# Kernel optimization log

Measured on AMD Instinct MI355X. Metric: run time of the kernel, lower is better.

## Reference

```python
import jax, jax.numpy as jnp
import numpy as np

N_NODES = 65536
N_EDGES = 524288
FEAT_DIM = 512
EMBED_DIM = 512


def setup_inputs() -> dict:
    key = jax.random.key(0)
    k1, k2, k3, k4, k5 = jax.random.split(key, 5)
    x = jax.random.normal(k1, (N_NODES, FEAT_DIM), dtype=jnp.float32)
    # xavier_uniform for (embed_dim, feat_dim)
    limit = float(np.sqrt(6.0 / (EMBED_DIM + FEAT_DIM)))
    weight = jax.random.uniform(k2, (EMBED_DIM, FEAT_DIM), dtype=jnp.float32,
                                minval=-limit, maxval=limit)
    row = jax.random.randint(k3, (N_EDGES,), 0, N_NODES, dtype=jnp.int64)
    col = jax.random.randint(k4, (N_EDGES,), 0, N_NODES, dtype=jnp.int64)
    vals = jax.random.uniform(k5, (N_EDGES,), dtype=jnp.float32)
    return {"x": x, "weight": weight, "row": row, "col": col, "vals": vals}


def reference(x, weight, row, col, vals):
    # Fused GEMM + SpMM: out = adj @ (x @ weight.T)
    h = jnp.einsum('nf,ef->ne', x, weight)            # [N, embed_dim] dense GEMM
    msgs = vals[:, None] * h[col]                     # [E, embed_dim] gather + scale
    out = jax.ops.segment_sum(msgs, row, num_segments=N_NODES)  # SpMM scatter-add
    return out
```

## Files before the change

kernel.cpp:

```cpp
#include <hip/hip_runtime.h>
#include <stdint.h>


#define N_NODES 65536
#define N_EDGES 524288
#define FEAT    512
#define EMB     512
#define CAP     64

typedef short  short8  __attribute__((ext_vector_type(8)));
typedef float  floatx4 __attribute__((ext_vector_type(4)));
typedef unsigned int uintx2 __attribute__((ext_vector_type(2)));

__device__ __forceinline__ unsigned short f2bf(float f) {
    unsigned int u = __float_as_uint(f);
    u += 0x7FFFu + ((u >> 16) & 1u);
    return (unsigned short)(u >> 16);
}
__device__ __forceinline__ float bf2f_lo(unsigned int u){ return __uint_as_float(u << 16); }
__device__ __forceinline__ float bf2f_hi(unsigned int u){ return __uint_as_float(u & 0xffff0000u); }

typedef __attribute__((address_space(1))) const void* gas_vp;
typedef __attribute__((address_space(3))) void*       las_vp;
#define GLDS16(g, l) __builtin_amdgcn_global_load_lds((gas_vp)(const void*)(g), (las_vp)(void*)(l), 16, 0, 0)

__global__ __launch_bounds__(256)
void conv_bf16(const float* __restrict__ in, unsigned short* __restrict__ out)
{
    size_t i = ((size_t)blockIdx.x * 256 + threadIdx.x) * 8;
    floatx4 a = __builtin_nontemporal_load((const floatx4*)&in[i]);
    floatx4 b = __builtin_nontemporal_load((const floatx4*)&in[i + 4]);
    ushort4 lo, hi;
    lo.x = f2bf(a.x); lo.y = f2bf(a.y); lo.z = f2bf(a.z); lo.w = f2bf(a.w);
    hi.x = f2bf(b.x); hi.y = f2bf(b.y); hi.z = f2bf(b.z); hi.w = f2bf(b.w);
    *(ushort4*)&out[i]     = lo;
    *(ushort4*)&out[i + 4] = hi;
}

__global__ __launch_bounds__(256)
void gemm_fast(const unsigned short* __restrict__ xb, const unsigned short* __restrict__ wb,
               unsigned short* __restrict__ h)
{
    __shared__ unsigned short As[128 * 64];
    __shared__ unsigned short Bs[128 * 64];

    const int t    = threadIdx.x;
    const int lane = t & 63;
    const int wave = t >> 6;
    const int wm   = wave >> 1;
    const int wn   = wave & 1;
    const int l15  = lane & 15;
    const int lq   = lane >> 4;

    const int xcd = blockIdx.x & 7;
    const int loc = blockIdx.x >> 3;
    const int m0  = (xcd * 64 + (loc >> 2)) * 128;
    const int n0  = (loc & 3) * 128;

    floatx4 acc[4][4];
    #pragma unroll
    for (int i = 0; i < 4; i++)
        #pragma unroll
        for (int j = 0; j < 4; j++) acc[i][j] = (floatx4){0.f, 0.f, 0.f, 0.f};

    const int r8 = t >> 3;
    const int c8 = t & 7;

    for (int kb = 0; kb < FEAT; kb += 64) {
        #pragma unroll
        for (int p = 0; p < 4; p++) {
            int row = p * 32 + r8;
            int lc  = c8 ^ (row & 7);
            GLDS16(&xb[(m0 + row) * FEAT + kb + lc * 8], &As[row * 64 + c8 * 8]);
            GLDS16(&wb[(n0 + row) * FEAT + kb + lc * 8], &Bs[row * 64 + c8 * 8]);
        }
        __syncthreads();
        #pragma unroll
        for (int kk = 0; kk < 2; kk++) {
            short8 af[4], bf[4];
            #pragma unroll
            for (int mt = 0; mt < 4; mt++) {
                int r  = wm * 64 + mt * 16 + l15;
                int pc = (kk * 4 + lq) ^ (r & 7);
                af[mt] = *(const short8*)&As[r * 64 + pc * 8];
            }
            #pragma unroll
            for (int nt = 0; nt < 4; nt++) {
                int r  = wn * 64 + nt * 16 + l15;
                int pc = (kk * 4 + lq) ^ (r & 7);
                bf[nt] = *(const short8*)&Bs[r * 64 + pc * 8];
            }
            #pragma unroll
            for (int mt = 0; mt < 4; mt++)
                #pragma unroll
                for (int nt = 0; nt < 4; nt++)
                    acc[mt][nt] = __builtin_amdgcn_mfma_f32_16x16x32_bf16(
                        af[mt], bf[nt], acc[mt][nt], 0, 0, 0);
        }
        __syncthreads();
    }

    #pragma unroll
    for (int mt = 0; mt < 4; mt++)
        #pragma unroll
        for (int nt = 0; nt < 4; nt++)
            #pragma unroll
            for (int r = 0; r < 4; r++) {
                int row = m0 + wm * 64 + mt * 16 + lq * 4 + r;
                int col = n0 + wn * 64 + nt * 16 + l15;
                h[row * EMB + col] = f2bf(acc[mt][nt][r]);
            }
}

#define BM 128
#define BN 64
#define LDA 72

__global__ __launch_bounds__(256)
void gemm_f32(const float* __restrict__ x, const float* __restrict__ w,
              unsigned short* __restrict__ h)
{
    __shared__ unsigned short As[BM][LDA];
    __shared__ unsigned short Bs[BN][LDA];

    const int t = threadIdx.x, lane = t & 63, wave = t >> 6;
    const int wm = wave >> 1, wn = wave & 1;
    const int l15 = lane & 15, lq = lane >> 4;
    const int xcd = blockIdx.x & 7;
    const int loc = blockIdx.x >> 3;
    const int m0 = (xcd * 64 + (loc >> 3)) * BM;
    const int n0 = (loc & 7) * BN;

    floatx4 acc[4][2];
    #pragma unroll
    for (int i = 0; i < 4; i++)
        #pragma unroll
        for (int j = 0; j < 2; j++) acc[i][j] = (floatx4){0.f, 0.f, 0.f, 0.f};

    for (int kb = 0; kb < FEAT; kb += 64) {
        #pragma unroll
        for (int p = 0; p < 8; p++) {
            int idx = p * 256 + t, row = idx >> 4, cv = (idx & 15) << 2;
            float4 v = *(const float4*)&x[(m0 + row) * FEAT + kb + cv];
            ushort4 b4 = {f2bf(v.x), f2bf(v.y), f2bf(v.z), f2bf(v.w)};
            *(ushort4*)&As[row][cv] = b4;
        }
        #pragma unroll
        for (int p = 0; p < 4; p++) {
            int idx = p * 256 + t, row = idx >> 4, cv = (idx & 15) << 2;
            float4 v = *(const float4*)&w[(n0 + row) * FEAT + kb + cv];
            ushort4 b4 = {f2bf(v.x), f2bf(v.y), f2bf(v.z), f2bf(v.w)};
            *(ushort4*)&Bs[row][cv] = b4;
        }
        __syncthreads();
        #pragma unroll
        for (int kk = 0; kk < 2; kk++) {
            short8 af[4], bf[2];
            #pragma unroll
            for (int mt = 0; mt < 4; mt++)
                af[mt] = *(const short8*)&As[wm * 64 + mt * 16 + l15][kk * 32 + lq * 8];
            #pragma unroll
            for (int nt = 0; nt < 2; nt++)
                bf[nt] = *(const short8*)&Bs[wn * 32 + nt * 16 + l15][kk * 32 + lq * 8];
            #pragma unroll
            for (int mt = 0; mt < 4; mt++)
                #pragma unroll
                for (int nt = 0; nt < 2; nt++)
                    acc[mt][nt] = __builtin_amdgcn_mfma_f32_16x16x32_bf16(
                        af[mt], bf[nt], acc[mt][nt], 0, 0, 0);
        }
        __syncthreads();
    }
    #pragma unroll
    for (int mt = 0; mt < 4; mt++)
        #pragma unroll
        for (int nt = 0; nt < 2; nt++)
            #pragma unroll
            for (int r = 0; r < 4; r++) {
                int row = m0 + wm * 64 + mt * 16 + lq * 4 + r;
                int col = n0 + wn * 32 + nt * 16 + l15;
                h[row * EMB + col] = f2bf(acc[mt][nt][r]);
            }
}

__global__ __launch_bounds__(256)
void fill_edges(const int* __restrict__ row, const int* __restrict__ col,
                const float* __restrict__ vals, int* __restrict__ cnt,
                uintx2* __restrict__ ebuf)
{
    int e = blockIdx.x * 256 + threadIdx.x;
    int   r = __builtin_nontemporal_load(&row[e]);
    int   c = __builtin_nontemporal_load(&col[e]);
    float v = __builtin_nontemporal_load(&vals[e]);
    int slot = atomicAdd(&cnt[r], 1);
    if (slot < CAP) {
        uintx2 ev; ev.x = (unsigned)c; ev.y = __float_as_uint(v);
        ebuf[r * CAP + slot] = ev;
    }
}

__global__ __launch_bounds__(256)
void rowsum(const unsigned short* __restrict__ h, const int* __restrict__ cnt,
            const uintx2* __restrict__ ebuf, float* __restrict__ out)
{
    const int r    = blockIdx.x * 4 + (threadIdx.x >> 6);
    const int lane = threadIdx.x & 63;
    int deg = cnt[r];
    if (deg > CAP) deg = CAP;
    const int base = r * CAP;

    int   c_l = 0;
    float v_l = 0.f;
    if (lane < deg) {
        uintx2 ev = ebuf[base + lane];
        c_l = (int)ev.x;
        v_l = __uint_as_float(ev.y);
    }

    float acc[8] = {0.f,0.f,0.f,0.f,0.f,0.f,0.f,0.f};
    for (int i0 = 0; i0 < deg; i0 += 8) {
        uint4 hv[8]; float vv[8];
        int nn = deg - i0; if (nn > 8) nn = 8;
        #pragma unroll
        for (int j = 0; j < 8; j++) {
            if (j < nn) {
                int c = __shfl(c_l, i0 + j, 64);
                vv[j] = __shfl(v_l, i0 + j, 64);
                hv[j] = *(const uint4*)&h[c * EMB + lane * 8];
            }
        }
        #pragma unroll
        for (int j = 0; j < 8; j++) {
            if (j < nn) {
                float v = vv[j];
                acc[0] += v * bf2f_lo(hv[j].x); acc[1] += v * bf2f_hi(hv[j].x);
                acc[2] += v * bf2f_lo(hv[j].y); acc[3] += v * bf2f_hi(hv[j].y);
                acc[4] += v * bf2f_lo(hv[j].z); acc[5] += v * bf2f_hi(hv[j].z);
                acc[6] += v * bf2f_lo(hv[j].w); acc[7] += v * bf2f_hi(hv[j].w);
            }
        }
    }
    floatx4* o = (floatx4*)&out[r * EMB + lane * 8];
    floatx4 o0; o0.x = acc[0]; o0.y = acc[1]; o0.z = acc[2]; o0.w = acc[3];
    floatx4 o1; o1.x = acc[4]; o1.y = acc[5]; o1.z = acc[6]; o1.w = acc[7];
    __builtin_nontemporal_store(o0, o);
    __builtin_nontemporal_store(o1, o + 1);
}

__global__ __launch_bounds__(128)
void scatter_atomic(const int* __restrict__ row, const int* __restrict__ col,
                    const float* __restrict__ vals, const unsigned short* __restrict__ h,
                    float* __restrict__ out)
{
    int e = blockIdx.x;
    int r = row[e], c = col[e];
    float v = vals[e];
    int f = threadIdx.x * 4;
    uint2 hv = *(const uint2*)&h[c * EMB + f];
    float* o = &out[r * EMB + f];
    atomicAdd(o + 0, v * bf2f_lo(hv.x));
    atomicAdd(o + 1, v * bf2f_hi(hv.x));
    atomicAdd(o + 2, v * bf2f_lo(hv.y));
    atomicAdd(o + 3, v * bf2f_hi(hv.y));
}

extern "C" void kernel_launch(void* const* d_in, const int* in_sizes, int n_in,
                              void* d_out, int out_size, void* d_ws, size_t ws_size,
                              hipStream_t stream) {
    const float* x    = (const float*)d_in[0];
    const float* w    = (const float*)d_in[1];
    const int*   row  = (const int*)d_in[2];
    const int*   col  = (const int*)d_in[3];
    const float* vals = (const float*)d_in[4];
    float* out = (float*)d_out;
    char* ws = (char*)d_ws;

    const size_t SZ_XB  = (size_t)N_NODES * FEAT * 2;
    const size_t SZ_WB  = (size_t)EMB * FEAT * 2;
    const size_t SZ_H   = (size_t)N_NODES * EMB * 2;
    const size_t SZ_CNT = (size_t)N_NODES * 4;
    const size_t SZ_E   = (size_t)N_NODES * CAP * 8;
    const size_t NEED_FAST = SZ_XB + SZ_WB + SZ_H + SZ_CNT;
    const size_t NEED_BIN  = SZ_H + SZ_CNT + SZ_E;

    if (ws_size >= NEED_FAST) {
        unsigned short* xb = (unsigned short*)ws;
        uintx2* ebuf = (uintx2*)ws;
        unsigned short* wb = (unsigned short*)(ws + SZ_XB);
        unsigned short* h  = (unsigned short*)(ws + SZ_XB + SZ_WB);
        int* cnt = (int*)(ws + SZ_XB + SZ_WB + SZ_H);

        conv_bf16<<<dim3((N_NODES * FEAT) / (256 * 8)), dim3(256), 0, stream>>>(x, xb);
        conv_bf16<<<dim3((EMB * FEAT) / (256 * 8)), dim3(256), 0, stream>>>(w, wb);
        gemm_fast<<<dim3(2048), dim3(256), 0, stream>>>(xb, wb, h);
        (void)hipMemsetAsync(cnt, 0, SZ_CNT, stream);
        fill_edges<<<dim3(N_EDGES / 256), dim3(256), 0, stream>>>(row, col, vals, cnt, ebuf);
        rowsum<<<dim3(N_NODES / 4), dim3(256), 0, stream>>>(h, cnt, ebuf, out);
    } else if (ws_size >= NEED_BIN) {
        unsigned short* h = (unsigned short*)ws;
        int*    cnt  = (int*)(ws + SZ_H);
        uintx2* ebuf = (uintx2*)(ws + SZ_H + SZ_CNT);

        gemm_f32<<<dim3(4096), dim3(256), 0, stream>>>(x, w, h);
        (void)hipMemsetAsync(cnt, 0, SZ_CNT, stream);
        fill_edges<<<dim3(N_EDGES / 256), dim3(256), 0, stream>>>(row, col, vals, cnt, ebuf);
        rowsum<<<dim3(N_NODES / 4), dim3(256), 0, stream>>>(h, cnt, ebuf, out);
    } else {
        unsigned short* h = (unsigned short*)ws;
        gemm_f32<<<dim3(4096), dim3(256), 0, stream>>>(x, w, h);
        (void)hipMemsetAsync(out, 0, (size_t)out_size * sizeof(float), stream);
        scatter_atomic<<<dim3(N_EDGES), dim3(128), 0, stream>>>(row, col, vals, h, out);
    }
}
```

Measured before the change: 384.4 us.

## Fuse x bf16 conversion into GEMM and process two rows per wave in rowsum

```diff
diff --git a/kernel.cpp b/kernel.cpp
--- a/kernel.cpp
+++ b/kernel.cpp
@@ -37,25 +37,23 @@
     *(ushort4*)&out[i + 4] = hi;
 }
 
-__global__ __launch_bounds__(256)
-void gemm_fast(const unsigned short* __restrict__ xb, const unsigned short* __restrict__ wb,
-               unsigned short* __restrict__ h)
-{
-    __shared__ unsigned short As[128 * 64];
-    __shared__ unsigned short Bs[128 * 64];
+__global__ __launch_bounds__(512, 4)
+void gemm_fused(const float* __restrict__ x, const unsigned short* __restrict__ wb,
+                unsigned short* __restrict__ h)
+{
+    __shared__ unsigned short As[64 * 64];
+    __shared__ unsigned short Bs[512 * 64];
 
     const int t    = threadIdx.x;
     const int lane = t & 63;
     const int wave = t >> 6;
-    const int wm   = wave >> 1;
-    const int wn   = wave & 1;
     const int l15  = lane & 15;
     const int lq   = lane >> 4;
 
-    const int xcd = blockIdx.x & 7;
-    const int loc = blockIdx.x >> 3;
-    const int m0  = (xcd * 64 + (loc >> 2)) * 128;
-    const int n0  = (loc & 3) * 128;
+    const int m0 = blockIdx.x * 64;
+
+    const int r8 = t >> 3;
+    const int c8 = t & 7;
 
     floatx4 acc[4][4];
     #pragma unroll
@@ -63,39 +61,57 @@
         #pragma unroll
         for (int j = 0; j < 4; j++) acc[i][j] = (floatx4){0.f, 0.f, 0.f, 0.f};
 
-    const int r8 = t >> 3;
-    const int c8 = t & 7;
+    float4 xa, xb_;
+    {
+        const float* px = &x[(size_t)(m0 + r8) * FEAT + c8 * 8];
+        xa  = *(const float4*)px;
+        xb_ = *(const float4*)(px + 4);
+    }
 
     for (int kb = 0; kb < FEAT; kb += 64) {
         #pragma unroll
-        for (int p = 0; p < 4; p++) {
-            int row = p * 32 + r8;
-            int lc  = c8 ^ (row & 7);
-            GLDS16(&xb[(m0 + row) * FEAT + kb + lc * 8], &As[row * 64 + c8 * 8]);
-            GLDS16(&wb[(n0 + row) * FEAT + kb + lc * 8], &Bs[row * 64 + c8 * 8]);
+        for (int p = 0; p < 8; p++) {
+            int row = p * 64 + r8;
+            int lc  = c8 ^ (r8 & 7);
+            GLDS16(&wb[row * FEAT + kb + lc * 8], &Bs[row * 64 + c8 * 8]);
+        }
+        {
+            short8 v;
+            v[0] = (short)f2bf(xa.x);  v[1] = (short)f2bf(xa.y);
+            v[2] = (short)f2bf(xa.z);  v[3] = (short)f2bf(xa.w);
+            v[4] = (short)f2bf(xb_.x); v[5] = (short)f2bf(xb_.y);
+            v[6] = (short)f2bf(xb_.z); v[7] = (short)f2bf(xb_.w);
+            *(short8*)&As[r8 * 64 + (c8 ^ (r8 & 7)) * 8] = v;
         }
         __syncthreads();
+
+        if (kb + 64 < FEAT) {
+            const float* px = &x[(size_t)(m0 + r8) * FEAT + (kb + 64) + c8 * 8];
+            xa  = *(const float4*)px;
+            xb_ = *(const float4*)(px + 4);
+        }
+
         #pragma unroll
         for (int kk = 0; kk < 2; kk++) {
-            short8 af[4], bf[4];
+            short8 af[4], bfr[4];
             #pragma unroll
             for (int mt = 0; mt < 4; mt++) {
-                int r  = wm * 64 + mt * 16 + l15;
+                int r  = mt * 16 + l15;
                 int pc = (kk * 4 + lq) ^ (r & 7);
                 af[mt] = *(const short8*)&As[r * 64 + pc * 8];
             }
             #pragma unroll
             for (int nt = 0; nt < 4; nt++) {
-                int r  = wn * 64 + nt * 16 + l15;
+                int r  = wave * 64 + nt * 16 + l15;
                 int pc = (kk * 4 + lq) ^ (r & 7);
-                bf[nt] = *(const short8*)&Bs[r * 64 + pc * 8];
+                bfr[nt] = *(const short8*)&Bs[r * 64 + pc * 8];
             }
             #pragma unroll
             for (int mt = 0; mt < 4; mt++)
                 #pragma unroll
                 for (int nt = 0; nt < 4; nt++)
                     acc[mt][nt] = __builtin_amdgcn_mfma_f32_16x16x32_bf16(
-                        af[mt], bf[nt], acc[mt][nt], 0, 0, 0);
+                        af[mt], bfr[nt], acc[mt][nt], 0, 0, 0);
         }
         __syncthreads();
     }
@@ -106,9 +122,9 @@
         for (int nt = 0; nt < 4; nt++)
             #pragma unroll
             for (int r = 0; r < 4; r++) {
-                int row = m0 + wm * 64 + mt * 16 + lq * 4 + r;
-                int col = n0 + wn * 64 + nt * 16 + l15;
-                h[row * EMB + col] = f2bf(acc[mt][nt][r]);
+                int row = m0 + mt * 16 + lq * 4 + r;
+                int col = wave * 64 + nt * 16 + l15;
+                h[(size_t)row * EMB + col] = f2bf(acc[mt][nt][r]);
             }
 }
 
@@ -203,48 +219,83 @@
 void rowsum(const unsigned short* __restrict__ h, const int* __restrict__ cnt,
             const uintx2* __restrict__ ebuf, float* __restrict__ out)
 {
-    const int r    = blockIdx.x * 4 + (threadIdx.x >> 6);
+    const int wid  = blockIdx.x * 4 + (threadIdx.x >> 6);
+    const int rA   = wid * 2;
+    const int rB   = rA + 1;
     const int lane = threadIdx.x & 63;
-    int deg = cnt[r];
-    if (deg > CAP) deg = CAP;
-    const int base = r * CAP;
-
-    int   c_l = 0;
-    float v_l = 0.f;
-    if (lane < deg) {
-        uintx2 ev = ebuf[base + lane];
-        c_l = (int)ev.x;
-        v_l = __uint_as_float(ev.y);
-    }
-
-    float acc[8] = {0.f,0.f,0.f,0.f,0.f,0.f,0.f,0.f};
-    for (int i0 = 0; i0 < deg; i0 += 8) {
-        uint4 hv[8]; float vv[8];
-        int nn = deg - i0; if (nn > 8) nn = 8;
+
+    int dA = cnt[rA]; if (dA > CAP) dA = CAP;
+    int dB = cnt[rB]; if (dB > CAP) dB = CAP;
+
+    int cA = 0, cB = 0; float vA = 0.f, vB = 0.f;
+    if (lane < dA) { uintx2 e = ebuf[rA * CAP + lane]; cA = (int)e.x; vA = __uint_as_float(e.y); }
+    if (lane < dB) { uintx2 e = ebuf[rB * CAP + lane]; cB = (int)e.x; vB = __uint_as_float(e.y); }
+
+    float accA[8] = {0.f,0.f,0.f,0.f,0.f,0.f,0.f,0.f};
+    float accB[8] = {0.f,0.f,0.f,0.f,0.f,0.f,0.f,0.f};
+
+    const int dMax  = dA > dB ? dA : dB;
+    const int iters = (dMax + 7) >> 3;
+
+    for (int it = 0; it < iters; it++) {
+        const int i0 = it * 8;
+        uint4 hA[8], hB[8];
+        float wA[8], wB[8];
+        int nA = dA - i0; if (nA > 8) nA = 8; if (nA < 0) nA = 0;
+        int nB = dB - i0; if (nB > 8) nB = 8; if (nB < 0) nB = 0;
+
         #pragma unroll
         for (int j = 0; j < 8; j++) {
-            if (j < nn) {
-                int c = __shfl(c_l, i0 + j, 64);
-                vv[j] = __shfl(v_l, i0 + j, 64);
-                hv[j] = *(const uint4*)&h[c * EMB + lane * 8];
+            if (j < nA) {
+                int c = __shfl(cA, i0 + j, 64);
+                wA[j] = __shfl(vA, i0 + j, 64);
+                hA[j] = *(const uint4*)&h[(size_t)c * EMB + lane * 8];
             }
         }
         #pragma unroll
         for (int j = 0; j < 8; j++) {
-            if (j < nn) {
-                float v = vv[j];
-                acc[0] += v * bf2f_lo(hv[j].x); acc[1] += v * bf2f_hi(hv[j].x);
-                acc[2] += v * bf2f_lo(hv[j].y); acc[3] += v * bf2f_hi(hv[j].y);
-                acc[4] += v * bf2f_lo(hv[j].z); acc[5] += v * bf2f_hi(hv[j].z);
-                acc[6] += v * bf2f_lo(hv[j].w); acc[7] += v * bf2f_hi(hv[j].w);
-            }
-        }
-    }
-    floatx4* o = (floatx4*)&out[r * EMB + lane * 8];
-    floatx4 o0; o0.x = acc[0]; o0.y = acc[1]; o0.z = acc[2]; o0.w = acc[3];
-    floatx4 o1; o1.x = acc[4]; o1.y = acc[5]; o1.z = acc[6]; o1.w = acc[7];
-    __builtin_nontemporal_store(o0, o);
-    __builtin_nontemporal_store(o1, o + 1);
+            if (j < nB) {
+                int c = __shfl(cB, i0 + j, 64);
+                wB[j] = __shfl(vB, i0 + j, 64);
+                hB[j] = *(const uint4*)&h[(size_t)c * EMB + lane * 8];
+            }
+        }
+        #pragma unroll
+        for (int j = 0; j < 8; j++) {
+            if (j < nA) {
+                float v = wA[j];
+                accA[0] += v * bf2f_lo(hA[j].x); accA[1] += v * bf2f_hi(hA[j].x);
+                accA[2] += v * bf2f_lo(hA[j].y); accA[3] += v * bf2f_hi(hA[j].y);
+                accA[4] += v * bf2f_lo(hA[j].z); accA[5] += v * bf2f_hi(hA[j].z);
+                accA[6] += v * bf2f_lo(hA[j].w); accA[7] += v * bf2f_hi(hA[j].w);
+            }
+        }
+        #pragma unroll
+        for (int j = 0; j < 8; j++) {
+            if (j < nB) {
+                float v = wB[j];
+                accB[0] += v * bf2f_lo(hB[j].x); accB[1] += v * bf2f_hi(hB[j].x);
+                accB[2] += v * bf2f_lo(hB[j].y); accB[3] += v * bf2f_hi(hB[j].y);
+                accB[4] += v * bf2f_lo(hB[j].z); accB[5] += v * bf2f_hi(hB[j].z);
+                accB[6] += v * bf2f_lo(hB[j].w); accB[7] += v * bf2f_hi(hB[j].w);
+            }
+        }
+    }
+
+    {
+        floatx4* o = (floatx4*)&out[(size_t)rA * EMB + lane * 8];
+        floatx4 o0; o0.x = accA[0]; o0.y = accA[1]; o0.z = accA[2]; o0.w = accA[3];
+        floatx4 o1; o1.x = accA[4]; o1.y = accA[5]; o1.z = accA[6]; o1.w = accA[7];
+        __builtin_nontemporal_store(o0, o);
+        __builtin_nontemporal_store(o1, o + 1);
+    }
+    {
+        floatx4* o = (floatx4*)&out[(size_t)rB * EMB + lane * 8];
+        floatx4 o0; o0.x = accB[0]; o0.y = accB[1]; o0.z = accB[2]; o0.w = accB[3];
+        floatx4 o1; o1.x = accB[4]; o1.y = accB[5]; o1.z = accB[6]; o1.w = accB[7];
+        __builtin_nontemporal_store(o0, o);
+        __builtin_nontemporal_store(o1, o + 1);
+    }
 }
 
 __global__ __launch_bounds__(128)
@@ -275,27 +326,24 @@
     float* out = (float*)d_out;
     char* ws = (char*)d_ws;
 
-    const size_t SZ_XB  = (size_t)N_NODES * FEAT * 2;
     const size_t SZ_WB  = (size_t)EMB * FEAT * 2;
     const size_t SZ_H   = (size_t)N_NODES * EMB * 2;
     const size_t SZ_CNT = (size_t)N_NODES * 4;
     const size_t SZ_E   = (size_t)N_NODES * CAP * 8;
-    const size_t NEED_FAST = SZ_XB + SZ_WB + SZ_H + SZ_CNT;
+    const size_t NEED_FAST = SZ_WB + SZ_H + SZ_CNT + SZ_E;
     const size_t NEED_BIN  = SZ_H + SZ_CNT + SZ_E;
 
     if (ws_size >= NEED_FAST) {
-        unsigned short* xb = (unsigned short*)ws;
-        uintx2* ebuf = (uintx2*)ws;
-        unsigned short* wb = (unsigned short*)(ws + SZ_XB);
-        unsigned short* h  = (unsigned short*)(ws + SZ_XB + SZ_WB);
-        int* cnt = (int*)(ws + SZ_XB + SZ_WB + SZ_H);
-
-        conv_bf16<<<dim3((N_NODES * FEAT) / (256 * 8)), dim3(256), 0, stream>>>(x, xb);
+        unsigned short* wb = (unsigned short*)ws;
+        unsigned short* h  = (unsigned short*)(ws + SZ_WB);
+        int*    cnt  = (int*)(ws + SZ_WB + SZ_H);
+        uintx2* ebuf = (uintx2*)(ws + SZ_WB + SZ_H + SZ_CNT);
+
         conv_bf16<<<dim3((EMB * FEAT) / (256 * 8)), dim3(256), 0, stream>>>(w, wb);
-        gemm_fast<<<dim3(2048), dim3(256), 0, stream>>>(xb, wb, h);
+        gemm_fused<<<dim3(N_NODES / 64), dim3(512), 0, stream>>>(x, wb, h);
         (void)hipMemsetAsync(cnt, 0, SZ_CNT, stream);
         fill_edges<<<dim3(N_EDGES / 256), dim3(256), 0, stream>>>(row, col, vals, cnt, ebuf);
-        rowsum<<<dim3(N_NODES / 4), dim3(256), 0, stream>>>(h, cnt, ebuf, out);
+        rowsum<<<dim3(N_NODES / 8), dim3(256), 0, stream>>>(h, cnt, ebuf, out);
     } else if (ws_size >= NEED_BIN) {
         unsigned short* h = (unsigned short*)ws;
         int*    cnt  = (int*)(ws + SZ_H);
@@ -304,7 +352,7 @@
         gemm_f32<<<dim3(4096), dim3(256), 0, stream>>>(x, w, h);
         (void)hipMemsetAsync(cnt, 0, SZ_CNT, stream);
         fill_edges<<<dim3(N_EDGES / 256), dim3(256), 0, stream>>>(row, col, vals, cnt, ebuf);
-        rowsum<<<dim3(N_NODES / 4), dim3(256), 0, stream>>>(h, cnt, ebuf, out);
+        rowsum<<<dim3(N_NODES / 8), dim3(256), 0, stream>>>(h, cnt, ebuf, out);
     } else {
         unsigned short* h = (unsigned short*)ws;
         gemm_f32<<<dim3(4096), dim3(256), 0, stream>>>(x, w, h);
```

New measurement: 400.3 us. +4.2%, slower.

## Fuse x bf16 conversion into GEMM and pad edge counters to separate cache lines

Applied to the files above, without the earlier changes.

```diff
diff --git a/kernel.cpp b/kernel.cpp
--- a/kernel.cpp
+++ b/kernel.cpp
@@ -7,6 +7,7 @@
 #define FEAT    512
 #define EMB     512
 #define CAP     64
+#define CNTS    16
 
 typedef short  short8  __attribute__((ext_vector_type(8)));
 typedef float  floatx4 __attribute__((ext_vector_type(4)));
@@ -37,25 +38,23 @@
     *(ushort4*)&out[i + 4] = hi;
 }
 
-__global__ __launch_bounds__(256)
-void gemm_fast(const unsigned short* __restrict__ xb, const unsigned short* __restrict__ wb,
-               unsigned short* __restrict__ h)
-{
-    __shared__ unsigned short As[128 * 64];
-    __shared__ unsigned short Bs[128 * 64];
+__global__ __launch_bounds__(512, 4)
+void gemm_fused(const float* __restrict__ x, const unsigned short* __restrict__ wb,
+                unsigned short* __restrict__ h)
+{
+    __shared__ unsigned short As[64 * 64];
+    __shared__ unsigned short Bs[512 * 64];
 
     const int t    = threadIdx.x;
     const int lane = t & 63;
     const int wave = t >> 6;
-    const int wm   = wave >> 1;
-    const int wn   = wave & 1;
     const int l15  = lane & 15;
     const int lq   = lane >> 4;
 
-    const int xcd = blockIdx.x & 7;
-    const int loc = blockIdx.x >> 3;
-    const int m0  = (xcd * 64 + (loc >> 2)) * 128;
-    const int n0  = (loc & 3) * 128;
+    const int m0 = blockIdx.x * 64;
+
+    const int r8 = t >> 3;
+    const int c8 = t & 7;
 
     floatx4 acc[4][4];
     #pragma unroll
@@ -63,39 +62,57 @@
         #pragma unroll
         for (int j = 0; j < 4; j++) acc[i][j] = (floatx4){0.f, 0.f, 0.f, 0.f};
 
-    const int r8 = t >> 3;
-    const int c8 = t & 7;
+    float4 xa, xb_;
+    {
+        const float* px = &x[(size_t)(m0 + r8) * FEAT + c8 * 8];
+        xa  = *(const float4*)px;
+        xb_ = *(const float4*)(px + 4);
+    }
 
     for (int kb = 0; kb < FEAT; kb += 64) {
         #pragma unroll
-        for (int p = 0; p < 4; p++) {
-            int row = p * 32 + r8;
-            int lc  = c8 ^ (row & 7);
-            GLDS16(&xb[(m0 + row) * FEAT + kb + lc * 8], &As[row * 64 + c8 * 8]);
-            GLDS16(&wb[(n0 + row) * FEAT + kb + lc * 8], &Bs[row * 64 + c8 * 8]);
+        for (int p = 0; p < 8; p++) {
+            int row = p * 64 + r8;
+            int lc  = c8 ^ (r8 & 7);
+            GLDS16(&wb[row * FEAT + kb + lc * 8], &Bs[row * 64 + c8 * 8]);
+        }
+        {
+            short8 v;
+            v[0] = (short)f2bf(xa.x);  v[1] = (short)f2bf(xa.y);
+            v[2] = (short)f2bf(xa.z);  v[3] = (short)f2bf(xa.w);
+            v[4] = (short)f2bf(xb_.x); v[5] = (short)f2bf(xb_.y);
+            v[6] = (short)f2bf(xb_.z); v[7] = (short)f2bf(xb_.w);
+            *(short8*)&As[r8 * 64 + (c8 ^ (r8 & 7)) * 8] = v;
         }
         __syncthreads();
+
+        if (kb + 64 < FEAT) {
+            const float* px = &x[(size_t)(m0 + r8) * FEAT + (kb + 64) + c8 * 8];
+            xa  = *(const float4*)px;
+            xb_ = *(const float4*)(px + 4);
+        }
+
         #pragma unroll
         for (int kk = 0; kk < 2; kk++) {
-            short8 af[4], bf[4];
+            short8 af[4], bfr[4];
             #pragma unroll
             for (int mt = 0; mt < 4; mt++) {
-                int r  = wm * 64 + mt * 16 + l15;
+                int r  = mt * 16 + l15;
                 int pc = (kk * 4 + lq) ^ (r & 7);
                 af[mt] = *(const short8*)&As[r * 64 + pc * 8];
             }
             #pragma unroll
             for (int nt = 0; nt < 4; nt++) {
-                int r  = wn * 64 + nt * 16 + l15;
+                int r  = wave * 64 + nt * 16 + l15;
                 int pc = (kk * 4 + lq) ^ (r & 7);
-                bf[nt] = *(const short8*)&Bs[r * 64 + pc * 8];
+                bfr[nt] = *(const short8*)&Bs[r * 64 + pc * 8];
             }
             #pragma unroll
             for (int mt = 0; mt < 4; mt++)
                 #pragma unroll
                 for (int nt = 0; nt < 4; nt++)
                     acc[mt][nt] = __builtin_amdgcn_mfma_f32_16x16x32_bf16(
-                        af[mt], bf[nt], acc[mt][nt], 0, 0, 0);
+                        af[mt], bfr[nt], acc[mt][nt], 0, 0, 0);
         }
         __syncthreads();
     }
@@ -106,9 +123,9 @@
         for (int nt = 0; nt < 4; nt++)
             #pragma unroll
             for (int r = 0; r < 4; r++) {
-                int row = m0 + wm * 64 + mt * 16 + lq * 4 + r;
-                int col = n0 + wn * 64 + nt * 16 + l15;
-                h[row * EMB + col] = f2bf(acc[mt][nt][r]);
+                int row = m0 + mt * 16 + lq * 4 + r;
+                int col = wave * 64 + nt * 16 + l15;
+                h[(size_t)row * EMB + col] = f2bf(acc[mt][nt][r]);
             }
 }
 
@@ -192,7 +209,7 @@
     int   r = __builtin_nontemporal_load(&row[e]);
     int   c = __builtin_nontemporal_load(&col[e]);
     float v = __builtin_nontemporal_load(&vals[e]);
-    int slot = atomicAdd(&cnt[r], 1);
+    int slot = atomicAdd(&cnt[(size_t)r * CNTS], 1);
     if (slot < CAP) {
         uintx2 ev; ev.x = (unsigned)c; ev.y = __float_as_uint(v);
         ebuf[r * CAP + slot] = ev;
@@ -201,11 +218,11 @@
 
 __global__ __launch_bounds__(256)
 void rowsum(const unsigned short* __restrict__ h, const int* __restrict__ cnt,
-            const uintx2* __restrict__ ebuf, float* __restrict__ out)
-{
-    const int r    = blockIdx.x * 4 + (threadIdx.x >> 6);
+            const uintx2* __restrict__ ebuf, float* __restrict__ out, int rbase)
+{
+    const int r    = rbase + blockIdx.x * 4 + (threadIdx.x >> 6);
     const int lane = threadIdx.x & 63;
-    int deg = cnt[r];
+    int deg = cnt[(size_t)r * CNTS];
     if (deg > CAP) deg = CAP;
     const int base = r * CAP;
 
@@ -226,7 +243,7 @@
             if (j < nn) {
                 int c = __shfl(c_l, i0 + j, 64);
                 vv[j] = __shfl(v_l, i0 + j, 64);
-                hv[j] = *(const uint4*)&h[c * EMB + lane * 8];
+                hv[j] = *(const uint4*)&h[(size_t)c * EMB + lane * 8];
             }
         }
         #pragma unroll
@@ -240,7 +257,7 @@
             }
         }
     }
-    floatx4* o = (floatx4*)&out[r * EMB + lane * 8];
+    floatx4* o = (floatx4*)&out[(size_t)r * EMB + lane * 8];
     floatx4 o0; o0.x = acc[0]; o0.y = acc[1]; o0.z = acc[2]; o0.w = acc[3];
     floatx4 o1; o1.x = acc[4]; o1.y = acc[5]; o1.z = acc[6]; o1.w = acc[7];
     __builtin_nontemporal_store(o0, o);
@@ -275,27 +292,25 @@
     float* out = (float*)d_out;
     char* ws = (char*)d_ws;
 
-    const size_t SZ_XB  = (size_t)N_NODES * FEAT * 2;
     const size_t SZ_WB  = (size_t)EMB * FEAT * 2;
     const size_t SZ_H   = (size_t)N_NODES * EMB * 2;
-    const size_t SZ_CNT = (size_t)N_NODES * 4;
+    const size_t SZ_CNT = (size_t)N_NODES * CNTS * 4;
     const size_t SZ_E   = (size_t)N_NODES * CAP * 8;
-    const size_t NEED_FAST = SZ_XB + SZ_WB + SZ_H + SZ_CNT;
+    const size_t NEED_FAST = SZ_WB + SZ_H + SZ_CNT + SZ_E;
     const size_t NEED_BIN  = SZ_H + SZ_CNT + SZ_E;
 
     if (ws_size >= NEED_FAST) {
-        unsigned short* xb = (unsigned short*)ws;
-        uintx2* ebuf = (uintx2*)ws;
-        unsigned short* wb = (unsigned short*)(ws + SZ_XB);
-        unsigned short* h  = (unsigned short*)(ws + SZ_XB + SZ_WB);
-        int* cnt = (int*)(ws + SZ_XB + SZ_WB + SZ_H);
-
-        conv_bf16<<<dim3((N_NODES * FEAT) / (256 * 8)), dim3(256), 0, stream>>>(x, xb);
+        unsigned short* wb = (unsigned short*)ws;
+        unsigned short* h  = (unsigned short*)(ws + SZ_WB);
+        int*    cnt  = (int*)(ws + SZ_WB + SZ_H);
+        uintx2* ebuf = (uintx2*)(ws + SZ_WB + SZ_H + SZ_CNT);
+
         conv_bf16<<<dim3((EMB * FEAT) / (256 * 8)), dim3(256), 0, stream>>>(w, wb);
-        gemm_fast<<<dim3(2048), dim3(256), 0, stream>>>(xb, wb, h);
+        gemm_fused<<<dim3(N_NODES / 64), dim3(512), 0, stream>>>(x, wb, h);
         (void)hipMemsetAsync(cnt, 0, SZ_CNT, stream);
         fill_edges<<<dim3(N_EDGES / 256), dim3(256), 0, stream>>>(row, col, vals, cnt, ebuf);
-        rowsum<<<dim3(N_NODES / 4), dim3(256), 0, stream>>>(h, cnt, ebuf, out);
+        rowsum<<<dim3(N_NODES / 8), dim3(256), 0, stream>>>(h, cnt, ebuf, out, 0);
+        rowsum<<<dim3(N_NODES / 8), dim3(256), 0, stream>>>(h, cnt, ebuf, out, N_NODES / 2);
     } else if (ws_size >= NEED_BIN) {
         unsigned short* h = (unsigned short*)ws;
         int*    cnt  = (int*)(ws + SZ_H);
@@ -304,7 +319,8 @@
         gemm_f32<<<dim3(4096), dim3(256), 0, stream>>>(x, w, h);
         (void)hipMemsetAsync(cnt, 0, SZ_CNT, stream);
         fill_edges<<<dim3(N_EDGES / 256), dim3(256), 0, stream>>>(row, col, vals, cnt, ebuf);
-        rowsum<<<dim3(N_NODES / 4), dim3(256), 0, stream>>>(h, cnt, ebuf, out);
+        rowsum<<<dim3(N_NODES / 8), dim3(256), 0, stream>>>(h, cnt, ebuf, out, 0);
+        rowsum<<<dim3(N_NODES / 8), dim3(256), 0, stream>>>(h, cnt, ebuf, out, N_NODES / 2);
     } else {
         unsigned short* h = (unsigned short*)ws;
         gemm_f32<<<dim3(4096), dim3(256), 0, stream>>>(x, w, h);
```

Result: no change. 388.8 us (+1.2%).
